# Performance work log

Measured on AMD Instinct MI355X. Metric: run time of the kernel, lower is better.

The kernel has to match this reference:

```python
import jax, jax.numpy as jnp
import numpy as np
from jax import lax

B, C_IN, C_OUT, KS, K, FD, L = 32, 128, 256, 9, 8, 64, 4096
PAD = KS // 2


def setup_inputs() -> dict:
    key = jax.random.key(0)
    ks = jax.random.split(key, 8)
    X = jax.random.normal(ks[0], (B, C_IN, L), dtype=jnp.float32)
    Z = jax.random.normal(ks[1], (B, FD), dtype=jnp.float32)
    # z_to_in: Linear(fluct_dim, in_planes), xavier-ish init, zero bias
    z_in_w = jax.random.normal(ks[2], (C_IN, FD), dtype=jnp.float32) * (1.0 / np.sqrt(FD))
    z_in_b = jnp.zeros((C_IN,), dtype=jnp.float32)
    # z_to_w MLP: in_planes -> in_planes//2 -> K
    w1 = jax.random.normal(ks[3], (C_IN // 2, C_IN), dtype=jnp.float32) * (1.0 / np.sqrt(C_IN))
    b1 = jax.random.normal(ks[4], (C_IN // 2,), dtype=jnp.float32) * 0.01
    w2 = jax.random.normal(ks[5], (K, C_IN // 2), dtype=jnp.float32) * (1.0 / np.sqrt(C_IN // 2))
    b2 = jax.random.normal(ks[6], (K,), dtype=jnp.float32) * 0.01
    weight_bank = jax.random.normal(ks[7], (K, C_OUT, C_IN, KS), dtype=jnp.float32) * (1.0 / np.sqrt(C_IN * KS))
    bias_bank = jnp.zeros((K, C_OUT), dtype=jnp.float32)
    return {"X": X, "Z": Z, "z_in_w": z_in_w, "z_in_b": z_in_b,
            "w1": w1, "b1": b1, "w2": w2, "b2": b2,
            "weight_bank": weight_bank, "bias_bank": bias_bank}


def _conv_one(x, w):
    # x: (C_in, L); w: (C_out, C_in, KS) -> (C_out, L)
    y = lax.conv_general_dilated(x[None], w, window_strides=(1,),
                                 padding=[(PAD, PAD)],
                                 dimension_numbers=("NCH", "OIH", "NCH"))
    return y[0]


def reference(X, Z, z_in_w, z_in_b, w1, b1, w2, b2, weight_bank, bias_bank):
    # routing: Z -> in_planes -> MLP -> softmax over K (dropout is inference no-op)
    proj = Z @ z_in_w.T + z_in_b                       # (B, C_in)
    h = jax.nn.relu(proj @ w1.T + b1)                  # (B, C_in//2)
    logits = h @ w2.T + b2                             # (B, K)
    omega = jax.nn.softmax(logits, axis=1)             # (B, K)
    # per-sample mixed kernels and biases
    W_tilde = jnp.einsum("bk,koci->boci", omega, weight_bank)  # (B, C_out, C_in, KS)
    b_tilde = omega @ bias_bank                         # (B, C_out)
    # batched per-sample conv (equiv. of the groups=B conv1d trick)
    Y = jax.vmap(_conv_one)(X, W_tilde)                 # (B, C_out, L)
    return Y + b_tilde[:, :, None]
```

## Files before the change

kernel.cpp:

```cpp
#include <hip/hip_runtime.h>
#include <math.h>

#define B_     32
#define C_INP  128
#define C_OUTP 256
#define KS_    9
#define KK_    8
#define FD_    64
#define LL_    4096
#define PAD_   4

#define LPAD   (LL_ + 2 * PAD_)

typedef unsigned short ushort_t;
typedef short bf16x8 __attribute__((ext_vector_type(8)));
typedef float f32x4 __attribute__((ext_vector_type(4)));

__device__ __forceinline__ ushort_t f2bf(float f) {
    unsigned u = __float_as_uint(f);
    unsigned r = (u + 0x7FFFu + ((u >> 16) & 1u)) >> 16;
    return (ushort_t)r;
}

__device__ __forceinline__ void gload16(const void* g, void* l) {
    __builtin_amdgcn_global_load_lds(
        (const __attribute__((address_space(1))) unsigned int*)g,
        (__attribute__((address_space(3))) unsigned int*)l, 16, 0, 0);
}

__global__ __launch_bounds__(256) void routing_kernel(
    const float* __restrict__ Z, const float* __restrict__ z_in_w,
    const float* __restrict__ z_in_b, const float* __restrict__ w1,
    const float* __restrict__ b1, const float* __restrict__ w2,
    const float* __restrict__ b2, const float* __restrict__ bias_bank,
    float* __restrict__ omega_out, float* __restrict__ btilde_out)
{
    const int b = blockIdx.x;
    const int tid = threadIdx.x;
    __shared__ float s_z[FD_];
    __shared__ float s_proj[C_INP];
    __shared__ float s_h[FD_];
    __shared__ float s_logits[KK_];
    __shared__ float s_omega[KK_];

    if (tid < FD_) s_z[tid] = Z[b * FD_ + tid];
    __syncthreads();

    if (tid < C_INP) {
        float acc = z_in_b[tid];
        const float* w = z_in_w + tid * FD_;
        #pragma unroll 8
        for (int f = 0; f < FD_; ++f) acc = fmaf(w[f], s_z[f], acc);
        s_proj[tid] = acc;
    }
    __syncthreads();

    if (tid < FD_) {
        float acc = b1[tid];
        const float* w = w1 + tid * C_INP;
        #pragma unroll 8
        for (int c = 0; c < C_INP; ++c) acc = fmaf(w[c], s_proj[c], acc);
        s_h[tid] = fmaxf(acc, 0.0f);
    }
    __syncthreads();

    if (tid < KK_) {
        float acc = b2[tid];
        const float* w = w2 + tid * FD_;
        #pragma unroll 8
        for (int j = 0; j < FD_; ++j) acc = fmaf(w[j], s_h[j], acc);
        s_logits[tid] = acc;
    }
    __syncthreads();

    if (tid == 0) {
        float m = s_logits[0];
        #pragma unroll
        for (int k = 1; k < KK_; ++k) m = fmaxf(m, s_logits[k]);
        float e[KK_];
        float s = 0.0f;
        #pragma unroll
        for (int k = 0; k < KK_; ++k) { e[k] = expf(s_logits[k] - m); s += e[k]; }
        const float inv = 1.0f / s;
        #pragma unroll
        for (int k = 0; k < KK_; ++k) s_omega[k] = e[k] * inv;
    }
    __syncthreads();

    if (tid < KK_) omega_out[b * KK_ + tid] = s_omega[tid];

    {
        float acc = 0.0f;
        #pragma unroll
        for (int k = 0; k < KK_; ++k) acc = fmaf(s_omega[k], bias_bank[k * C_OUTP + tid], acc);
        btilde_out[b * C_OUTP + tid] = acc;
    }
}

__global__ __launch_bounds__(256) void mix_kernel(
    const float* __restrict__ bank, const float* __restrict__ omega,
    ushort_t* __restrict__ wt)
{
    __shared__ float s_bank[KK_ * C_INP * KS_];
    __shared__ float s_om[B_ * KK_];

    const int o = blockIdx.x;
    const int tid = threadIdx.x;

    s_om[tid] = omega[tid];
    #pragma unroll
    for (int k = 0; k < KK_; ++k) {
        const float* src = bank + ((size_t)(k * C_OUTP + o)) * (C_INP * KS_);
        for (int i = tid; i < C_INP * KS_; i += 256)
            s_bank[k * (C_INP * KS_) + i] = src[i];
    }
    __syncthreads();

    for (int j = tid; j < KS_ * (C_INP / 2); j += 256) {
        const int t = j >> 6;
        const int c = (j & 63) * 2;
        float v0[KK_], v1[KK_];
        #pragma unroll
        for (int k = 0; k < KK_; ++k) {
            v0[k] = s_bank[k * (C_INP * KS_) + c * KS_ + t];
            v1[k] = s_bank[k * (C_INP * KS_) + (c + 1) * KS_ + t];
        }
        #pragma unroll
        for (int b = 0; b < B_; ++b) {
            float a0 = 0.0f, a1 = 0.0f;
            #pragma unroll
            for (int k = 0; k < KK_; ++k) {
                const float om = s_om[b * KK_ + k];
                a0 = fmaf(om, v0[k], a0);
                a1 = fmaf(om, v1[k], a1);
            }
            const unsigned packed = (unsigned)f2bf(a0) | ((unsigned)f2bf(a1) << 16);
            *(unsigned*)&wt[(((size_t)b * KS_ + t) * C_OUTP + o) * C_INP + c] = packed;
        }
    }
}

__global__ __launch_bounds__(256) void transpose_kernel(
    const float* __restrict__ X, ushort_t* __restrict__ XT)
{
    __shared__ ushort_t s_t[64 * 130];

    const int tid = threadIdx.x;
    const int l0 = blockIdx.x * 64;
    const int b = blockIdx.y;

    const int ll = tid & 63;
    const int cq = tid >> 6;
    const float* xb = X + ((size_t)b * C_INP) * LL_;

    #pragma unroll 4
    for (int r = 0; r < 32; ++r) {
        const int c = r * 4 + cq;
        s_t[ll * 130 + c] = f2bf(xb[(size_t)c * LL_ + l0 + ll]);
    }
    __syncthreads();

    ushort_t* xtb = XT + (size_t)b * LPAD * C_INP;
    for (int it = tid; it < 64 * 64; it += 256) {
        const int row = it >> 6;
        const int p = it & 63;
        const unsigned lo = s_t[row * 130 + p * 2];
        const unsigned hi = s_t[row * 130 + p * 2 + 1];
        *(unsigned*)(xtb + ((size_t)(4 + l0 + row)) * C_INP + p * 2) = lo | (hi << 16);
    }
    if (l0 == 0) {
        const int row = tid >> 6, p = tid & 63;
        *(unsigned*)(xtb + (size_t)row * C_INP + p * 2) = 0u;
    }
    if (l0 == LL_ - 64) {
        const int row = tid >> 6, p = tid & 63;
        *(unsigned*)(xtb + ((size_t)(LL_ + PAD_ + row)) * C_INP + p * 2) = 0u;
    }
}

__global__ __launch_bounds__(512, 2) void gemm_kernel(
    const ushort_t* __restrict__ XT, const ushort_t* __restrict__ WT,
    const float* __restrict__ btilde, float* __restrict__ Y)
{
    __shared__ __align__(16) ushort_t sX[264 * 128];
    __shared__ __align__(16) ushort_t sWr[4][256 * 32];

    const int tid = threadIdx.x;
    const int wid = tid >> 6;
    const int lane = tid & 63;

    const int wg = blockIdx.x;
    const int logical = (wg & 7) * 64 + (wg >> 3);
    const int b  = logical >> 4;
    const int l0 = (logical & 15) << 8;

    const ushort_t* xtb = XT + ((size_t)b * LPAD + l0) * C_INP;
    const ushort_t* wtb = WT + (size_t)b * KS_ * C_OUTP * C_INP;

    for (int g = tid; g < 4224; g += 512) {
        const int row = g >> 4;
        const int pcp = g & 15;
        gload16(xtb + row * C_INP + ((pcp ^ (row & 7)) * 8), sX + g * 8);
    }
    #pragma unroll
    for (int p = 0; p < 3; ++p) {
        ushort_t* wd = sWr[p];
        const ushort_t* wsp = wtb + p * 32;
        #pragma unroll
        for (int itr = 0; itr < 2; ++itr) {
            const int g = itr * 512 + tid;
            gload16(wsp + (g >> 2) * C_INP + (g & 3) * 8, wd + g * 8);
        }
    }
    __syncthreads();

    const int ln15 = lane & 15;
    const int lh = lane >> 4;
    const int wm0 = (wid >> 2) * 128;
    const int wn0 = (wid & 3) * 64;

    f32x4 acc[8][4];
    #pragma unroll
    for (int i = 0; i < 8; ++i)
        #pragma unroll
        for (int j = 0; j < 4; ++j) acc[i][j] = (f32x4){0.f, 0.f, 0.f, 0.f};

    #pragma unroll 1
    for (int hs = 0; hs < 36; ++hs) {
        const int t = hs >> 2;
        const int q = hs & 3;
        int hs2 = hs + 3; if (hs2 >= 36) hs2 -= 36;
        const int t2 = hs2 >> 2;
        const int q2 = hs2 & 3;
        const ushort_t* wr = sWr[hs & 3];
        ushort_t* wdst = sWr[hs2 & 3];
        const ushort_t* wsrc = wtb + ((size_t)t2 * C_OUTP) * C_INP + q2 * 32;

        bf16x8 a[8], bx[4];

        #pragma unroll
        for (int i = 0; i < 4; ++i) {
            const int arow = wm0 + i * 16 + ln15;
            a[i] = *(const bf16x8*)&wr[arow * 32 + lh * 8];
        }
        #pragma unroll
        for (int j = 0; j < 4; ++j) {
            const int brow = wn0 + t + j * 16 + ln15;
            const int pcx = (q * 4 + lh) ^ (brow & 7);
            bx[j] = *(const bf16x8*)&sX[brow * 128 + pcx * 8];
        }
        {
            const int g = tid;
            gload16(wsrc + (g >> 2) * C_INP + (g & 3) * 8, wdst + g * 8);
        }
        __builtin_amdgcn_s_barrier();
        __builtin_amdgcn_s_setprio(1);
        #pragma unroll
        for (int i = 0; i < 4; ++i)
            #pragma unroll
            for (int j = 0; j < 4; ++j)
                acc[i][j] = __builtin_amdgcn_mfma_f32_16x16x32_bf16(
                    a[i], bx[j], acc[i][j], 0, 0, 0);
        __builtin_amdgcn_s_setprio(0);

        #pragma unroll
        for (int i = 4; i < 8; ++i) {
            const int arow = wm0 + i * 16 + ln15;
            a[i] = *(const bf16x8*)&wr[arow * 32 + lh * 8];
        }
        {
            const int g = 512 + tid;
            gload16(wsrc + (g >> 2) * C_INP + (g & 3) * 8, wdst + g * 8);
        }
        __builtin_amdgcn_s_barrier();
        __builtin_amdgcn_s_setprio(1);
        #pragma unroll
        for (int i = 4; i < 8; ++i)
            #pragma unroll
            for (int j = 0; j < 4; ++j)
                acc[i][j] = __builtin_amdgcn_mfma_f32_16x16x32_bf16(
                    a[i], bx[j], acc[i][j], 0, 0, 0);
        __builtin_amdgcn_s_setprio(0);

        asm volatile("s_waitcnt vmcnt(4)" ::: "memory");
        __builtin_amdgcn_s_barrier();
        __builtin_amdgcn_sched_barrier(0);
    }
    asm volatile("s_waitcnt vmcnt(0)" ::: "memory");

    #pragma unroll
    for (int i = 0; i < 8; ++i) {
        const int obase = wm0 + i * 16 + lh * 4;
        const float4 bt = *(const float4*)&btilde[b * C_OUTP + obase];
        #pragma unroll
        for (int j = 0; j < 4; ++j) {
            const int lcol = l0 + wn0 + j * 16 + ln15;
            float* yp = Y + ((size_t)(b * C_OUTP + obase)) * LL_ + lcol;
            yp[0]           = acc[i][j][0] + bt.x;
            yp[LL_]         = acc[i][j][1] + bt.y;
            yp[2 * LL_]     = acc[i][j][2] + bt.z;
            yp[3 * LL_]     = acc[i][j][3] + bt.w;
        }
    }
}

#define O_TILE 8
#define T_PAD  12
__global__ __launch_bounds__(256) void conv_kernel(
    const float* __restrict__ X, const float* __restrict__ bank,
    const float* __restrict__ omega, const float* __restrict__ btilde,
    float* __restrict__ Y)
{
    __shared__ __align__(16) float s_w[C_INP * O_TILE * T_PAD];
    __shared__ float s_om[KK_];

    const int tid = threadIdx.x;
    const int o_base = blockIdx.x * O_TILE;
    const int b = blockIdx.y;

    if (tid < KK_) s_om[tid] = omega[b * KK_ + tid];
    __syncthreads();

    {
        const size_t kstride = (size_t)C_OUTP * C_INP * KS_;
        const float* bank_base = bank + (size_t)o_base * C_INP * KS_;
        for (int idx = tid; idx < O_TILE * C_INP * KS_; idx += 256) {
            const int o = idx / (C_INP * KS_);
            const int rem = idx - o * (C_INP * KS_);
            const int c = rem / KS_;
            const int t = rem - c * KS_;
            const float* p = bank_base + idx;
            float acc = 0.0f;
            #pragma unroll
            for (int k = 0; k < KK_; ++k) acc = fmaf(s_om[k], p[k * kstride], acc);
            s_w[(c * O_TILE + o) * T_PAD + t] = acc;
        }
    }
    __syncthreads();

    const int og = tid >> 7;
    const int lg = tid & 127;
    const float* xb = X + (size_t)b * C_INP * LL_;

    float bt[4];
    #pragma unroll
    for (int o = 0; o < 4; ++o) bt[o] = btilde[b * C_OUTP + o_base + og * 4 + o];

    for (int it = 0; it < 4; ++it) {
        const int l0 = it * 1024 + lg * 8;
        const int lx = l0 - PAD_;
        const bool fast = (lx >= 0) && (lx + 16 <= LL_);

        float acc[4][8];
        #pragma unroll
        for (int o = 0; o < 4; ++o)
            #pragma unroll
            for (int j = 0; j < 8; ++j) acc[o][j] = 0.0f;

        #pragma unroll 1
        for (int c = 0; c < C_INP; ++c) {
            const float* xrow = xb + (size_t)c * LL_;
            float x[16];
            if (fast) {
                const float4* p = reinterpret_cast<const float4*>(xrow + lx);
                const float4 a0 = p[0], a1 = p[1], a2 = p[2], a3 = p[3];
                x[0]=a0.x; x[1]=a0.y; x[2]=a0.z; x[3]=a0.w;
                x[4]=a1.x; x[5]=a1.y; x[6]=a1.z; x[7]=a1.w;
                x[8]=a2.x; x[9]=a2.y; x[10]=a2.z; x[11]=a2.w;
                x[12]=a3.x; x[13]=a3.y; x[14]=a3.z; x[15]=a3.w;
            } else {
                #pragma unroll
                for (int j = 0; j < 16; ++j) {
                    const int q = lx + j;
                    x[j] = (q >= 0 && q < LL_) ? xrow[q] : 0.0f;
                }
            }
            const float* wp = &s_w[(c * O_TILE + og * 4) * T_PAD];
            #pragma unroll
            for (int o = 0; o < 4; ++o) {
                #pragma unroll
                for (int t = 0; t < KS_; ++t) {
                    const float wv = wp[o * T_PAD + t];
                    #pragma unroll
                    for (int j = 0; j < 8; ++j)
                        acc[o][j] = fmaf(wv, x[j + t], acc[o][j]);
                }
            }
        }

        float* yb = Y + ((size_t)(b * C_OUTP + o_base + og * 4)) * LL_ + l0;
        #pragma unroll
        for (int o = 0; o < 4; ++o) {
            float4 r0, r1;
            r0.x = acc[o][0] + bt[o]; r0.y = acc[o][1] + bt[o];
            r0.z = acc[o][2] + bt[o]; r0.w = acc[o][3] + bt[o];
            r1.x = acc[o][4] + bt[o]; r1.y = acc[o][5] + bt[o];
            r1.z = acc[o][6] + bt[o]; r1.w = acc[o][7] + bt[o];
            float4* yp = reinterpret_cast<float4*>(yb + (size_t)o * LL_);
            yp[0] = r0; yp[1] = r1;
        }
    }
}

extern "C" void kernel_launch(void* const* d_in, const int* in_sizes, int n_in,
                              void* d_out, int out_size, void* d_ws, size_t ws_size,
                              hipStream_t stream)
{
    const float* X         = (const float*)d_in[0];
    const float* Z         = (const float*)d_in[1];
    const float* z_in_w    = (const float*)d_in[2];
    const float* z_in_b    = (const float*)d_in[3];
    const float* w1        = (const float*)d_in[4];
    const float* b1        = (const float*)d_in[5];
    const float* w2        = (const float*)d_in[6];
    const float* b2        = (const float*)d_in[7];
    const float* bank      = (const float*)d_in[8];
    const float* bias_bank = (const float*)d_in[9];
    float* out = (float*)d_out;

    char* ws = (char*)d_ws;
    float* omega  = (float*)ws;
    float* btilde = (float*)(ws + 1024);
    ushort_t* wt  = (ushort_t*)(ws + 1024 + 32768);
    ushort_t* XT  = (ushort_t*)(ws + 1024 + 32768 + (size_t)B_ * KS_ * C_OUTP * C_INP * 2);
    const size_t WS_NEEDED = 1024 + 32768
        + (size_t)B_ * KS_ * C_OUTP * C_INP * 2
        + (size_t)B_ * LPAD * C_INP * 2;

    routing_kernel<<<B_, 256, 0, stream>>>(Z, z_in_w, z_in_b, w1, b1, w2, b2,
                                           bias_bank, omega, btilde);

    if (ws_size >= WS_NEEDED) {
        mix_kernel<<<C_OUTP, 256, 0, stream>>>(bank, omega, wt);
        transpose_kernel<<<dim3(LL_ / 64, B_), 256, 0, stream>>>(X, XT);
        gemm_kernel<<<512, 512, 0, stream>>>(XT, wt, btilde, out);
    } else {
        dim3 grid(C_OUTP / O_TILE, B_);
        conv_kernel<<<grid, 256, 0, stream>>>(X, bank, omega, btilde, out);
    }
}
```

Baseline: 131.2 us.

## Load GEMM weight fragments directly from global into registers, dropping LDS ring

Removes the 4-stage LDS ring buffer for the mixed weights and the per-step barriers. Each wave now loads its A fragments straight from global memory into registers, double-buffered across two register sets. The wave tiling changes from 128x64 to 64x128 (output channels by positions), so each A fragment is reused across 8 X columns and fewer weight bytes are fetched per MFMA. This saves LDS space and synchronization, but it exposes global load latency. Its only cover is one step of register prefetch, and each lane reads scattered 16-byte pieces at row stride.

New measurement: 145.0 us. 10.5% more time.

```diff
diff --git a/kernel.cpp b/kernel.cpp
--- a/kernel.cpp
+++ b/kernel.cpp
@@ -183,7 +183,6 @@
     const float* __restrict__ btilde, float* __restrict__ Y)
 {
     __shared__ __align__(16) ushort_t sX[264 * 128];
-    __shared__ __align__(16) ushort_t sWr[4][256 * 32];
 
     const int tid = threadIdx.x;
     const int wid = tid >> 6;
@@ -202,98 +201,71 @@
         const int pcp = g & 15;
         gload16(xtb + row * C_INP + ((pcp ^ (row & 7)) * 8), sX + g * 8);
     }
-    #pragma unroll
-    for (int p = 0; p < 3; ++p) {
-        ushort_t* wd = sWr[p];
-        const ushort_t* wsp = wtb + p * 32;
-        #pragma unroll
-        for (int itr = 0; itr < 2; ++itr) {
-            const int g = itr * 512 + tid;
-            gload16(wsp + (g >> 2) * C_INP + (g & 3) * 8, wd + g * 8);
-        }
-    }
     __syncthreads();
 
     const int ln15 = lane & 15;
     const int lh = lane >> 4;
-    const int wm0 = (wid >> 2) * 128;
-    const int wn0 = (wid & 3) * 64;
-
-    f32x4 acc[8][4];
+    const int wm0 = (wid >> 1) * 64;
+    const int wn0 = (wid & 1) * 128;
+
+    const ushort_t* abase = wtb + (size_t)(wm0 + ln15) * C_INP + lh * 8;
+
+    f32x4 acc[4][8];
     #pragma unroll
-    for (int i = 0; i < 8; ++i)
-        #pragma unroll
-        for (int j = 0; j < 4; ++j) acc[i][j] = (f32x4){0.f, 0.f, 0.f, 0.f};
+    for (int i = 0; i < 4; ++i)
+        #pragma unroll
+        for (int j = 0; j < 8; ++j) acc[i][j] = (f32x4){0.f, 0.f, 0.f, 0.f};
+
+    #define LOADA(dst, hsv)                                                    \
+        {                                                                      \
+            const int t_ = (hsv) >> 2, q_ = (hsv) & 3;                         \
+            const ushort_t* p_ = abase + (size_t)t_ * (C_OUTP * C_INP) + q_ * 32; \
+            dst##0 = *(const bf16x8*)(p_);                                     \
+            dst##1 = *(const bf16x8*)(p_ + 16 * C_INP);                        \
+            dst##2 = *(const bf16x8*)(p_ + 32 * C_INP);                        \
+            dst##3 = *(const bf16x8*)(p_ + 48 * C_INP);                        \
+        }
+
+    #define COMPUTE(areg, hsv)                                                 \
+        {                                                                      \
+            const int t_ = (hsv) >> 2, q_ = (hsv) & 3;                         \
+            bf16x8 bx[8];                                                      \
+            _Pragma("unroll")                                                  \
+            for (int j = 0; j < 8; ++j) {                                      \
+                const int brow = wn0 + t_ + j * 16 + ln15;                     \
+                const int pcx = (q_ * 4 + lh) ^ (brow & 7);                    \
+                bx[j] = *(const bf16x8*)&sX[brow * 128 + pcx * 8];             \
+            }                                                                  \
+            _Pragma("unroll")                                                  \
+            for (int j = 0; j < 8; ++j) {                                      \
+                acc[0][j] = __builtin_amdgcn_mfma_f32_16x16x32_bf16(areg##0, bx[j], acc[0][j], 0, 0, 0); \
+                acc[1][j] = __builtin_amdgcn_mfma_f32_16x16x32_bf16(areg##1, bx[j], acc[1][j], 0, 0, 0); \
+                acc[2][j] = __builtin_amdgcn_mfma_f32_16x16x32_bf16(areg##2, bx[j], acc[2][j], 0, 0, 0); \
+                acc[3][j] = __builtin_amdgcn_mfma_f32_16x16x32_bf16(areg##3, bx[j], acc[3][j], 0, 0, 0); \
+            }                                                                  \
+        }
+
+    bf16x8 aP0, aP1, aP2, aP3, aQ0, aQ1, aQ2, aQ3;
+    LOADA(aP, 0)
 
     #pragma unroll 1
-    for (int hs = 0; hs < 36; ++hs) {
-        const int t = hs >> 2;
-        const int q = hs & 3;
-        int hs2 = hs + 3; if (hs2 >= 36) hs2 -= 36;
-        const int t2 = hs2 >> 2;
-        const int q2 = hs2 & 3;
-        const ushort_t* wr = sWr[hs & 3];
-        ushort_t* wdst = sWr[hs2 & 3];
-        const ushort_t* wsrc = wtb + ((size_t)t2 * C_OUTP) * C_INP + q2 * 32;
-
-        bf16x8 a[8], bx[4];
-
-        #pragma unroll
-        for (int i = 0; i < 4; ++i) {
-            const int arow = wm0 + i * 16 + ln15;
-            a[i] = *(const bf16x8*)&wr[arow * 32 + lh * 8];
-        }
-        #pragma unroll
-        for (int j = 0; j < 4; ++j) {
-            const int brow = wn0 + t + j * 16 + ln15;
-            const int pcx = (q * 4 + lh) ^ (brow & 7);
-            bx[j] = *(const bf16x8*)&sX[brow * 128 + pcx * 8];
-        }
-        {
-            const int g = tid;
-            gload16(wsrc + (g >> 2) * C_INP + (g & 3) * 8, wdst + g * 8);
-        }
-        __builtin_amdgcn_s_barrier();
-        __builtin_amdgcn_s_setprio(1);
-        #pragma unroll
-        for (int i = 0; i < 4; ++i)
-            #pragma unroll
-            for (int j = 0; j < 4; ++j)
-                acc[i][j] = __builtin_amdgcn_mfma_f32_16x16x32_bf16(
-                    a[i], bx[j], acc[i][j], 0, 0, 0);
-        __builtin_amdgcn_s_setprio(0);
-
-        #pragma unroll
-        for (int i = 4; i < 8; ++i) {
-            const int arow = wm0 + i * 16 + ln15;
-            a[i] = *(const bf16x8*)&wr[arow * 32 + lh * 8];
-        }
-        {
-            const int g = 512 + tid;
-            gload16(wsrc + (g >> 2) * C_INP + (g & 3) * 8, wdst + g * 8);
-        }
-        __builtin_amdgcn_s_barrier();
-        __builtin_amdgcn_s_setprio(1);
-        #pragma unroll
-        for (int i = 4; i < 8; ++i)
-            #pragma unroll
-            for (int j = 0; j < 4; ++j)
-                acc[i][j] = __builtin_amdgcn_mfma_f32_16x16x32_bf16(
-                    a[i], bx[j], acc[i][j], 0, 0, 0);
-        __builtin_amdgcn_s_setprio(0);
-
-        asm volatile("s_waitcnt vmcnt(4)" ::: "memory");
-        __builtin_amdgcn_s_barrier();
-        __builtin_amdgcn_sched_barrier(0);
-    }
-    asm volatile("s_waitcnt vmcnt(0)" ::: "memory");
+    for (int hs = 0; hs < 36; hs += 2) {
+        LOADA(aQ, hs + 1)
+        COMPUTE(aP, hs)
+        const int hs2 = (hs + 2 < 36) ? hs + 2 : 0;
+        LOADA(aP, hs2)
+        COMPUTE(aQ, hs + 1)
+    }
+
+    #undef LOADA
+    #undef COMPUTE
 
     #pragma unroll
-    for (int i = 0; i < 8; ++i) {
+    for (int i = 0; i < 4; ++i) {
         const int obase = wm0 + i * 16 + lh * 4;
         const float4 bt = *(const float4*)&btilde[b * C_OUTP + obase];
         #pragma unroll
-        for (int j = 0; j < 4; ++j) {
+        for (int j = 0; j < 8; ++j) {
             const int lcol = l0 + wn0 + j * 16 + ln15;
             float* yp = Y + ((size_t)(b * C_OUTP + obase)) * LL_ + lcol;
             yp[0]           = acc[i][j][0] + bt.x;
```

## Switch conv GEMM to 32x32x16 MFMA with swizzled weight LDS layout

Applied to the files above, without the earlier changes.

Replaces the 16x16x32 bf16 MFMA tiling with 32x32x16 MFMAs (4x2 fragments of 32x32 per wave), which cuts LDS fragment reads per FLOP and the number of MFMA issues. It also applies an XOR swizzle to the weight tiles in LDS to avoid bank conflicts. The two half-step barriers are merged into one loop body that issues all next-stage weight loads up front. The epilogue is remapped to the 32x32 accumulator layout, and the larger fragments raise register pressure.

Result: slower. 150.3 us (+14.5%).

```diff
diff --git a/kernel.cpp b/kernel.cpp
--- a/kernel.cpp
+++ b/kernel.cpp
@@ -15,6 +15,7 @@
 typedef unsigned short ushort_t;
 typedef short bf16x8 __attribute__((ext_vector_type(8)));
 typedef float f32x4 __attribute__((ext_vector_type(4)));
+typedef float f32x16 __attribute__((ext_vector_type(16)));
 
 __device__ __forceinline__ ushort_t f2bf(float f) {
     unsigned u = __float_as_uint(f);
@@ -209,77 +210,70 @@
         #pragma unroll
         for (int itr = 0; itr < 2; ++itr) {
             const int g = itr * 512 + tid;
-            gload16(wsp + (g >> 2) * C_INP + (g & 3) * 8, wd + g * 8);
-        }
-    }
-    __syncthreads();
-
-    const int ln15 = lane & 15;
-    const int lh = lane >> 4;
+            const int row = g >> 2;
+            const int sp = g & 3;
+            gload16(wsp + row * C_INP + ((sp ^ ((row >> 1) & 3)) * 8), wd + g * 8);
+        }
+    }
+    __syncthreads();
+
+    const int l31 = lane & 31;
+    const int lh2 = lane >> 5;
     const int wm0 = (wid >> 2) * 128;
     const int wn0 = (wid & 3) * 64;
 
-    f32x4 acc[8][4];
+    f32x16 acc[4][2];
     #pragma unroll
-    for (int i = 0; i < 8; ++i)
-        #pragma unroll
-        for (int j = 0; j < 4; ++j) acc[i][j] = (f32x4){0.f, 0.f, 0.f, 0.f};
+    for (int i = 0; i < 4; ++i)
+        #pragma unroll
+        for (int j = 0; j < 2; ++j)
+            acc[i][j] = (f32x16)(0.0f);
 
     #pragma unroll 1
-    for (int hs = 0; hs < 36; ++hs) {
-        const int t = hs >> 2;
-        const int q = hs & 3;
-        int hs2 = hs + 3; if (hs2 >= 36) hs2 -= 36;
-        const int t2 = hs2 >> 2;
-        const int q2 = hs2 & 3;
-        const ushort_t* wr = sWr[hs & 3];
-        ushort_t* wdst = sWr[hs2 & 3];
-        const ushort_t* wsrc = wtb + ((size_t)t2 * C_OUTP) * C_INP + q2 * 32;
-
-        bf16x8 a[8], bx[4];
-
-        #pragma unroll
-        for (int i = 0; i < 4; ++i) {
-            const int arow = wm0 + i * 16 + ln15;
-            a[i] = *(const bf16x8*)&wr[arow * 32 + lh * 8];
-        }
-        #pragma unroll
-        for (int j = 0; j < 4; ++j) {
-            const int brow = wn0 + t + j * 16 + ln15;
-            const int pcx = (q * 4 + lh) ^ (brow & 7);
-            bx[j] = *(const bf16x8*)&sX[brow * 128 + pcx * 8];
-        }
-        {
-            const int g = tid;
-            gload16(wsrc + (g >> 2) * C_INP + (g & 3) * 8, wdst + g * 8);
-        }
-        __builtin_amdgcn_s_barrier();
+    for (int s = 0; s < 36; ++s) {
+        const int t = s >> 2;
+        const int q = s & 3;
+        int s3 = s + 3; if (s3 >= 36) s3 -= 36;
+        const ushort_t* wr = sWr[s & 3];
+        ushort_t* wdst = sWr[s3 & 3];
+        const ushort_t* wsrc = wtb + (size_t)(s3 >> 2) * (C_OUTP * C_INP) + (s3 & 3) * 32;
+
+        #pragma unroll
+        for (int itr = 0; itr < 2; ++itr) {
+            const int g = itr * 512 + tid;
+            const int row = g >> 2;
+            const int sp = g & 3;
+            gload16(wsrc + row * C_INP + ((sp ^ ((row >> 1) & 3)) * 8), wdst + g * 8);
+        }
+
+        bf16x8 a[4][2], bx[2][2];
+        #pragma unroll
+        for (int mf = 0; mf < 4; ++mf) {
+            const int arow = wm0 + mf * 32 + l31;
+            const int xr = (arow >> 1) & 3;
+            #pragma unroll
+            for (int ks = 0; ks < 2; ++ks)
+                a[mf][ks] = *(const bf16x8*)&wr[arow * 32 + (((ks * 2 + lh2) ^ xr) << 3)];
+        }
+        #pragma unroll
+        for (int nf = 0; nf < 2; ++nf) {
+            const int brow = wn0 + t + nf * 32 + l31;
+            #pragma unroll
+            for (int ks = 0; ks < 2; ++ks) {
+                const int sl = (q * 4 + ks * 2 + lh2) ^ (brow & 7);
+                bx[nf][ks] = *(const bf16x8*)&sX[brow * 128 + sl * 8];
+            }
+        }
+
         __builtin_amdgcn_s_setprio(1);
         #pragma unroll
-        for (int i = 0; i < 4; ++i)
-            #pragma unroll
-            for (int j = 0; j < 4; ++j)
-                acc[i][j] = __builtin_amdgcn_mfma_f32_16x16x32_bf16(
-                    a[i], bx[j], acc[i][j], 0, 0, 0);
-        __builtin_amdgcn_s_setprio(0);
-
-        #pragma unroll
-        for (int i = 4; i < 8; ++i) {
-            const int arow = wm0 + i * 16 + ln15;
-            a[i] = *(const bf16x8*)&wr[arow * 32 + lh * 8];
-        }
-        {
-            const int g = 512 + tid;
-            gload16(wsrc + (g >> 2) * C_INP + (g & 3) * 8, wdst + g * 8);
-        }
-        __builtin_amdgcn_s_barrier();
-        __builtin_amdgcn_s_setprio(1);
-        #pragma unroll
-        for (int i = 4; i < 8; ++i)
-            #pragma unroll
-            for (int j = 0; j < 4; ++j)
-                acc[i][j] = __builtin_amdgcn_mfma_f32_16x16x32_bf16(
-                    a[i], bx[j], acc[i][j], 0, 0, 0);
+        for (int ks = 0; ks < 2; ++ks)
+            #pragma unroll
+            for (int mf = 0; mf < 4; ++mf)
+                #pragma unroll
+                for (int nf = 0; nf < 2; ++nf)
+                    acc[mf][nf] = __builtin_amdgcn_mfma_f32_32x32x16_bf16(
+                        a[mf][ks], bx[nf][ks], acc[mf][nf], 0, 0, 0);
         __builtin_amdgcn_s_setprio(0);
 
         asm volatile("s_waitcnt vmcnt(4)" ::: "memory");
@@ -289,17 +283,20 @@
     asm volatile("s_waitcnt vmcnt(0)" ::: "memory");
 
     #pragma unroll
-    for (int i = 0; i < 8; ++i) {
-        const int obase = wm0 + i * 16 + lh * 4;
-        const float4 bt = *(const float4*)&btilde[b * C_OUTP + obase];
-        #pragma unroll
-        for (int j = 0; j < 4; ++j) {
-            const int lcol = l0 + wn0 + j * 16 + ln15;
-            float* yp = Y + ((size_t)(b * C_OUTP + obase)) * LL_ + lcol;
-            yp[0]           = acc[i][j][0] + bt.x;
-            yp[LL_]         = acc[i][j][1] + bt.y;
-            yp[2 * LL_]     = acc[i][j][2] + bt.z;
-            yp[3 * LL_]     = acc[i][j][3] + bt.w;
+    for (int mf = 0; mf < 4; ++mf) {
+        const int rbase = wm0 + mf * 32 + 4 * lh2;
+        #pragma unroll
+        for (int rq = 0; rq < 4; ++rq) {
+            const float4 bt = *(const float4*)&btilde[b * C_OUTP + rbase + 8 * rq];
+            #pragma unroll
+            for (int nf = 0; nf < 2; ++nf) {
+                const int col = l0 + wn0 + nf * 32 + l31;
+                float* yp = Y + ((size_t)(b * C_OUTP + rbase + 8 * rq)) * LL_ + col;
+                yp[0]        = acc[mf][nf][rq * 4 + 0] + bt.x;
+                yp[LL_]      = acc[mf][nf][rq * 4 + 1] + bt.y;
+                yp[2 * LL_]  = acc[mf][nf][rq * 4 + 2] + bt.z;
+                yp[3 * LL_]  = acc[mf][nf][rq * 4 + 3] + bt.w;
+            }
         }
     }
 }
```
